# Kernel optimization log

Measured on AMD Instinct MI355X. Metric: run time of the kernel, lower is better.

The kernel has to match this reference:

```python
import jax, jax.numpy as jnp
import numpy as np

CLASSES = (16, 16)
CH_IN = 128
CH_LAT = 128
B, H, W = 1, 192, 256


def setup_inputs() -> dict:
    key = jax.random.key(0)
    ks = jax.random.split(key, 20)

    def w(k, shape, fan_in):
        return (jax.random.normal(k, shape, jnp.float32) / np.float32(np.sqrt(fan_in)))

    c0, c1 = CLASSES
    inp = {
        "x_in": jax.random.normal(ks[0], (B, CH_IN, H, W), jnp.float32),
        # 1x1 convs: weight [out, in], bias [out]
        "w_c11": w(ks[1], (CH_LAT, CH_IN), CH_IN), "b_c11": 0.01 * jax.random.normal(ks[2], (CH_LAT,), jnp.float32),
        "w_c12": w(ks[3], (CH_LAT, CH_LAT), CH_LAT), "b_c12": 0.01 * jax.random.normal(ks[4], (CH_LAT,), jnp.float32),
        "w_c13": w(ks[5], (c0 + 1, CH_LAT), CH_LAT), "b_c13": 0.01 * jax.random.normal(ks[6], (c0 + 1,), jnp.float32),
        # CondMul: weight [n_classes, in, out], bias [n_classes, out]
        "w_c21": w(ks[7], (c0, CH_IN, 32), CH_IN), "b_c21": 0.01 * jax.random.normal(ks[8], (c0, 32), jnp.float32),
        "w_c22": w(ks[9], (c0, 32, 32), 32), "b_c22": 0.01 * jax.random.normal(ks[10], (c0, 32), jnp.float32),
        "w_c23": w(ks[11], (c0, 32, c1), 32), "b_c23": 0.01 * jax.random.normal(ks[12], (c0, c1), jnp.float32),
        "w_r11": w(ks[13], (c0 * c1, CH_IN, 32), CH_IN), "b_r11": 0.01 * jax.random.normal(ks[14], (c0 * c1, 32), jnp.float32),
        "w_r12": w(ks[15], (c0 * c1, 32, 16), 32), "b_r12": 0.01 * jax.random.normal(ks[16], (c0 * c1, 16), jnp.float32),
        "w_r13": w(ks[17], (c0 * c1, 16, 1), 16), "b_r13": 0.01 * jax.random.normal(ks[18], (c0 * c1, 1), jnp.float32),
    }
    return inp


def _conv1x1(x, w, b):
    # x: [B,C,H,W], w: [O,C] -> [B,O,H,W]
    return jnp.einsum('bchw,oc->bohw', x, w) + b[None, :, None, None]


def _cond_mul(x, inds, w, b):
    # x: [N,in], inds: [N] int32, w: [C,in,out], b: [C,out] -> [N,out]
    return jnp.einsum('ni,nio->no', x, w[inds]) + b[inds]


def reference(x_in, w_c11, b_c11, w_c12, b_c12, w_c13, b_c13,
              w_c21, b_c21, w_c22, b_c22, w_c23, b_c23,
              w_r11, b_r11, w_r12, b_r12, w_r13, b_r13):
    lrelu = jax.nn.leaky_relu  # negative_slope=0.01, matches F.leaky_relu default
    c0, c1 = CLASSES
    total = c0 * c1

    x1 = lrelu(_conv1x1(x_in, w_c11, b_c11))
    x1 = lrelu(_conv1x1(x1, w_c12, b_c12))
    x1 = _conv1x1(x1, w_c13, b_c13)  # [B, c0+1, H, W]
    mask = lrelu(x1[:, -1:, :, :])

    # coarse routing: argmax over class logits, flattened in (B,H,W) order as in torch
    inds1 = jnp.argmax(x1[:, :c0], axis=1).reshape(-1).astype(jnp.int32)

    # tokens flattened via transpose(1,3): (B,W,H) order, faithful to original
    tok = jnp.transpose(x_in, (0, 3, 2, 1)).reshape(-1, x_in.shape[1])  # [N, CH_IN]

    x2 = lrelu(_cond_mul(tok, inds1, w_c21, b_c21))
    x2 = lrelu(_cond_mul(x2, inds1, w_c22, b_c22))
    x2 = _cond_mul(x2, inds1, w_c23, b_c23)  # [N, c1]

    inds2 = jnp.argmax(x2, axis=1).astype(jnp.int32)
    inds12 = inds1 * c0 + inds2  # original multiplies by classes[0]

    x3 = lrelu(_cond_mul(tok, inds12, w_r11, b_r11))
    x3 = lrelu(_cond_mul(x3, inds12, w_r12, b_r12))
    r = _cond_mul(x3, inds12, w_r13, b_r13).reshape(-1)  # [N]

    x_real = (inds12.astype(jnp.float32) + r) * (1.0 / float(total))
    x_real = x_real.reshape(x_in.shape[0], 1, x_in.shape[2], x_in.shape[3])
    return x_real, mask
```

## Files before the change

### kernel.cpp

```cpp
#include <hip/hip_runtime.h>

#define NPIX 49152
#define H_ 192
#define W_ 256
#define TPB 64

__global__ __launch_bounds__(256) void wtrans2_k(const float* __restrict__ Wa,
    float* __restrict__ WTa, const float* __restrict__ Wb,
    float* __restrict__ WTb, int* __restrict__ S) {
  const int b = blockIdx.x;
  const float* __restrict__ W = (b < 16) ? Wa : Wb;
  float* __restrict__ WT = (b < 16) ? WTa : WTb;
  const int bb = b & 15;
  __shared__ float tile[32][33];
  const int bx = bb & 3, by = bb >> 2;
  const int c = threadIdx.x & 31, r0 = threadIdx.x >> 5;
#pragma unroll
  for (int j = 0; j < 4; ++j) {
    const int r = r0 + j * 8;
    tile[r][c] = W[(by * 32 + r) * 128 + bx * 32 + c];
  }
  __syncthreads();
#pragma unroll
  for (int j = 0; j < 4; ++j) {
    const int r = r0 + j * 8;
    WT[(bx * 32 + r) * 128 + by * 32 + c] = tile[c][r];
  }
  if (b == 0) {
    const int t = threadIdx.x;
    if (t < 32) S[t] = 0;
    S[1088 + t] = 0;
    S[1344 + t] = 0;
  }
}

__global__ __launch_bounds__(512) void convfused_k(const float* __restrict__ X,
    const float* __restrict__ WT1, const float* __restrict__ Bv1,
    const float* __restrict__ WT2, const float* __restrict__ Bv2,
    const float* __restrict__ W3, const float* __restrict__ Bv3,
    unsigned char* __restrict__ inds1, float* __restrict__ mask_out,
    int* __restrict__ cnt1, float* __restrict__ xt) {
  __shared__ float xs2[128][65];
  __shared__ float w3s[128 * 20];
  __shared__ int lh[16];
  const int t = threadIdx.x;
  const int px = t & 63;
  const int p0 = blockIdx.x * 64;
  int ob = (t >> 6) * 16;
  ob = __builtin_amdgcn_readfirstlane(ob);
  if (t < 16) lh[t] = 0;

  {
    float xr[16];
#pragma unroll
    for (int kk = 0; kk < 16; ++kk)
      xr[kk] = X[(ob + kk) * NPIX + p0 + px];
#pragma unroll
    for (int kk = 0; kk < 16; ++kk)
      xs2[ob + kk][px] = xr[kk];
  }
  __syncthreads();

  float acc[16];

  const float* __restrict__ W1u = WT1 + ob;
#pragma unroll
  for (int o = 0; o < 16; ++o) acc[o] = Bv1[ob + o];
#pragma unroll 8
  for (int k = 0; k < 128; ++k) {
    const float xv = xs2[k][px];
#pragma unroll
    for (int o = 0; o < 16; ++o)
      acc[o] = fmaf(xv, W1u[k * 128 + o], acc[o]);
  }

#pragma unroll
  for (int i = 0; i < 4; ++i) {
    const int idx = t * 4 + i;
    const int tok = idx >> 5, c4 = idx & 31;
    const int pg = p0 + tok;
    float4 v;
    v.x = xs2[c4 * 4 + 0][tok];
    v.y = xs2[c4 * 4 + 1][tok];
    v.z = xs2[c4 * 4 + 2][tok];
    v.w = xs2[c4 * 4 + 3][tok];
    *(float4*)(xt + ((pg & 255) * H_ + (pg >> 8)) * 128 + c4 * 4) = v;
  }
  __syncthreads();

#pragma unroll
  for (int o = 0; o < 16; ++o) {
    const float v = acc[o];
    xs2[ob + o][px] = v > 0.f ? v : 0.01f * v;
  }
  __syncthreads();

  const float* __restrict__ W2u = WT2 + ob;
#pragma unroll
  for (int o = 0; o < 16; ++o) acc[o] = Bv2[ob + o];
#pragma unroll 8
  for (int k = 0; k < 128; ++k) {
    const float xv = xs2[k][px];
#pragma unroll
    for (int o = 0; o < 16; ++o)
      acc[o] = fmaf(xv, W2u[k * 128 + o], acc[o]);
  }
  __syncthreads();

#pragma unroll
  for (int o = 0; o < 16; ++o) {
    const float v = acc[o];
    xs2[ob + o][px] = v > 0.f ? v : 0.01f * v;
  }
  for (int i = t; i < 17 * 128; i += 512)
    w3s[(i & 127) * 20 + (i >> 7)] = W3[i];
  __syncthreads();

  {
    const int p = t >> 3, s = t & 7;
    float s2[2];
    s2[0] = Bv3[2 * s];
    s2[1] = Bv3[2 * s + 1];
    float m = Bv3[16];
#pragma unroll 8
    for (int k = 0; k < 128; ++k) {
      const float xv = xs2[k][p];
      float2 w2 = *(const float2*)&w3s[k * 20 + 2 * s];
      s2[0] = fmaf(xv, w2.x, s2[0]);
      s2[1] = fmaf(xv, w2.y, s2[1]);
      m = fmaf(xv, w3s[k * 20 + 16], m);
    }
    float bv = s2[0];
    int bi = 2 * s;
    if (s2[1] > bv) { bv = s2[1]; bi = 2 * s + 1; }
#pragma unroll
    for (int d = 1; d < 8; d <<= 1) {
      const float ov = __shfl_xor(bv, d, 64);
      const int oi = __shfl_xor(bi, d, 64);
      if (ov > bv || (ov == bv && oi < bi)) { bv = ov; bi = oi; }
    }
    if (s == 0) {
      inds1[p0 + p] = (unsigned char)bi;
      mask_out[p0 + p] = m > 0.f ? m : 0.01f * m;
      atomicAdd(&lh[bi], 1);
    }
  }
  __syncthreads();
  if (t < 16 && lh[t] > 0) atomicAdd(&cnt1[t], lh[t]);
}

template<typename T>
__global__ __launch_bounds__(256) void scatter_k(const T* __restrict__ bins,
    const int* __restrict__ cnt, int* __restrict__ cursor,
    int* __restrict__ ord, int nbins) {
  __shared__ int loff[256], lhist[256], lbase[256], lcur[256];
  __shared__ int wsC[4];
  const int t = threadIdx.x;
  const int lane = t & 63, wvi = t >> 6;
  const int c = (t < nbins) ? cnt[t] : 0;
  int ic = c;
  for (int d = 1; d < 64; d <<= 1) {
    const int u = __shfl_up(ic, d, 64);
    if (lane >= d) ic += u;
  }
  if (lane == 63) wsC[wvi] = ic;
  if (t < nbins) { lhist[t] = 0; lcur[t] = 0; }
  __syncthreads();
  int bc = 0;
#pragma unroll
  for (int w2 = 0; w2 < 4; ++w2) if (w2 < wvi) bc += wsC[w2];
  ic += bc;
  if (t < nbins) loff[t] = ic - c;
  __syncthreads();
  const int n = blockIdx.x * 256 + t;
  const int b = (int)bins[n];
  atomicAdd(&lhist[b], 1);
  __syncthreads();
  if (t < nbins && lhist[t] > 0) lbase[t] = atomicAdd(&cursor[t], lhist[t]);
  __syncthreads();
  const int r = atomicAdd(&lcur[b], 1);
  ord[loff[b] + lbase[b] + r] = n;
}

__global__ __launch_bounds__(256) void chain1_k(const float* __restrict__ xt,
    const int* __restrict__ ord1, const int* __restrict__ cnt1,
    const float* __restrict__ wc21, const float* __restrict__ bc21,
    const float* __restrict__ wc22, const float* __restrict__ bc22,
    const float* __restrict__ wc23, const float* __restrict__ bc23,
    int* __restrict__ e12a, int* __restrict__ cnt2) {
  __shared__ float w1s[4096];
  __shared__ float w2s[1024];
  __shared__ float w3s[512];
  __shared__ float bs[80];
  __shared__ float xs_[64][132];
  __shared__ int lh[16];
  __shared__ int sel[4];
  __shared__ int wsC[4], wsD[4];
  const int t = threadIdx.x;
  const int lane = t & 63, wvi = t >> 6;
  if (t == 0) sel[0] = -1;
  if (t < 16) lh[t] = 0;
  {
    const int cb = (t < 16) ? cnt1[t] : 0;
    const int nb = (cb + TPB - 1) / TPB;
    int ic = cb, id = nb;
    for (int d = 1; d < 64; d <<= 1) {
      const int uc = __shfl_up(ic, d, 64);
      const int ud = __shfl_up(id, d, 64);
      if (lane >= d) { ic += uc; id += ud; }
    }
    if (lane == 63) { wsC[wvi] = ic; wsD[wvi] = id; }
    __syncthreads();
    int bc = 0, bd = 0;
#pragma unroll
    for (int w2 = 0; w2 < 4; ++w2) {
      if (w2 < wvi) { bc += wsC[w2]; bd += wsD[w2]; }
    }
    ic += bc; id += bd;
    const int accB = id - nb, accO = ic - cb;
    if (t < 16 && (int)blockIdx.x >= accB && (int)blockIdx.x < accB + nb) {
      sel[0] = t; sel[1] = blockIdx.x - accB; sel[2] = accO; sel[3] = cb;
    }
  }
  __syncthreads();
  if (sel[0] < 0) return;
  const int e     = __builtin_amdgcn_readfirstlane(sel[0]);
  const int chunk = __builtin_amdgcn_readfirstlane(sel[1]);
  const int offe  = __builtin_amdgcn_readfirstlane(sel[2]);
  const int cnt   = __builtin_amdgcn_readfirstlane(sel[3]);

  const int tg = t >> 2, sub = t & 3;
  const int l0 = (t & 63) & ~3;
  const int pos = chunk * TPB + tg;
  const bool valid = pos < cnt;
  const int n = valid ? ord1[offe + pos] : 0;

  {
    const float4* __restrict__ Wg1 = (const float4*)(wc21 + e * 4096);
#pragma unroll
    for (int j = 0; j < 4; ++j)
      *(float4*)&w1s[t * 4 + j * 1024] = Wg1[t + j * 256];
    const float4* __restrict__ Wg2 = (const float4*)(wc22 + e * 1024);
    *(float4*)&w2s[t * 4] = Wg2[t];
    if (t < 128) {
      const float4* __restrict__ Wg3 = (const float4*)(wc23 + e * 512);
      *(float4*)&w3s[t * 4] = Wg3[t];
    }
    if (t < 32) bs[t] = bc21[e * 32 + t];
    else if (t < 64) bs[t] = bc22[e * 32 + (t - 32)];
    else if (t < 80) bs[t] = bc23[e * 16 + (t - 64)];
  }
  {
    const float4* __restrict__ src = (const float4*)(xt + n * 128 + sub * 32);
    float4 tmp[8];
#pragma unroll
    for (int j = 0; j < 8; ++j) tmp[j] = src[j];
#pragma unroll
    for (int j = 0; j < 8; ++j)
      *(float4*)(&xs_[tg][sub * 32 + 4 * j]) = tmp[j];
  }
  __syncthreads();

  const int wb1 = sub * 8;
  float a[8];
#pragma unroll
  for (int o = 0; o < 8; ++o) a[o] = bs[wb1 + o];
#pragma unroll
  for (int k = 0; k < 128; k += 4) {
    float x4[4];
    *(float4*)x4 = *(const float4*)(&xs_[tg][k]);
#pragma unroll
    for (int kk = 0; kk < 4; ++kk) {
      float w8[8];
      *(float4*)&w8[0] = *(const float4*)&w1s[(k + kk) * 32 + wb1];
      *(float4*)&w8[4] = *(const float4*)&w1s[(k + kk) * 32 + wb1 + 4];
#pragma unroll
      for (int o = 0; o < 8; ++o) a[o] = fmaf(x4[kk], w8[o], a[o]);
    }
  }
#pragma unroll
  for (int o = 0; o < 8; ++o) a[o] = a[o] > 0.f ? a[o] : 0.01f * a[o];

  float b[8];
#pragma unroll
  for (int o = 0; o < 8; ++o) b[o] = bs[32 + wb1 + o];
#pragma unroll
  for (int i = 0; i < 32; ++i) {
    const float hv = __shfl(a[i & 7], l0 + (i >> 3), 64);
    float w8[8];
    *(float4*)&w8[0] = *(const float4*)&w2s[i * 32 + wb1];
    *(float4*)&w8[4] = *(const float4*)&w2s[i * 32 + wb1 + 4];
#pragma unroll
    for (int o = 0; o < 8; ++o) b[o] = fmaf(hv, w8[o], b[o]);
  }
#pragma unroll
  for (int o = 0; o < 8; ++o) b[o] = b[o] > 0.f ? b[o] : 0.01f * b[o];

  float s[4];
#pragma unroll
  for (int j = 0; j < 4; ++j) s[j] = bs[64 + sub * 4 + j];
#pragma unroll
  for (int i = 0; i < 32; ++i) {
    const float hv = __shfl(b[i & 7], l0 + (i >> 3), 64);
    float w4[4];
    *(float4*)w4 = *(const float4*)&w3s[i * 16 + sub * 4];
#pragma unroll
    for (int j = 0; j < 4; ++j) s[j] = fmaf(hv, w4[j], s[j]);
  }

  float bv = s[0];
  int bi = sub * 4;
#pragma unroll
  for (int j = 1; j < 4; ++j) {
    if (s[j] > bv) { bv = s[j]; bi = sub * 4 + j; }
  }
#pragma unroll
  for (int d = 1; d < 4; d <<= 1) {
    const float ov = __shfl_xor(bv, d, 64);
    const int oi = __shfl_xor(bi, d, 64);
    if (ov > bv || (ov == bv && oi < bi)) { bv = ov; bi = oi; }
  }
  const int e12 = e * 16 + bi;
  if (valid && sub == 0) {
    e12a[n] = e12;
    atomicAdd(&lh[bi], 1);
  }
  __syncthreads();
  if (t < 16 && lh[t] > 0)
    atomicAdd(&cnt2[e * 16 + t], lh[t]);
}

__global__ __launch_bounds__(256) void chain2_k(const float* __restrict__ xt,
    const int* __restrict__ ord2, const int* __restrict__ cnt2,
    const float* __restrict__ wr11, const float* __restrict__ br11,
    const float* __restrict__ wr12, const float* __restrict__ br12,
    const float* __restrict__ wr13, const float* __restrict__ br13,
    float* __restrict__ out) {
  __shared__ float w1s[4096];
  __shared__ float w2s[512];
  __shared__ float w3s[16];
  __shared__ float bs[49];
  __shared__ float xs_[64][132];
  __shared__ int sel[4];
  __shared__ int wsC[4], wsD[4];
  const int t = threadIdx.x;
  const int lane = t & 63, wvi = t >> 6;
  if (t == 0) sel[0] = -1;
  {
    const int cb = cnt2[t];
    const int nb = (cb + TPB - 1) / TPB;
    int ic = cb, id = nb;
    for (int d = 1; d < 64; d <<= 1) {
      const int uc = __shfl_up(ic, d, 64);
      const int ud = __shfl_up(id, d, 64);
      if (lane >= d) { ic += uc; id += ud; }
    }
    if (lane == 63) { wsC[wvi] = ic; wsD[wvi] = id; }
    __syncthreads();
    int bc = 0, bd = 0;
#pragma unroll
    for (int w2 = 0; w2 < 4; ++w2) {
      if (w2 < wvi) { bc += wsC[w2]; bd += wsD[w2]; }
    }
    ic += bc; id += bd;
    const int accB = id - nb, accO = ic - cb;
    if ((int)blockIdx.x >= accB && (int)blockIdx.x < accB + nb) {
      sel[0] = t; sel[1] = blockIdx.x - accB; sel[2] = accO; sel[3] = cb;
    }
  }
  __syncthreads();
  if (sel[0] < 0) return;
  const int e12   = __builtin_amdgcn_readfirstlane(sel[0]);
  const int chunk = __builtin_amdgcn_readfirstlane(sel[1]);
  const int offe  = __builtin_amdgcn_readfirstlane(sel[2]);
  const int cnt   = __builtin_amdgcn_readfirstlane(sel[3]);

  const int tg = t >> 2, sub = t & 3;
  const int l0 = (t & 63) & ~3;
  const int pos = chunk * TPB + tg;
  const bool valid = pos < cnt;
  const int n = valid ? ord2[offe + pos] : 0;

  {
    const float4* __restrict__ Wg1 = (const float4*)(wr11 + e12 * 4096);
#pragma unroll
    for (int j = 0; j < 4; ++j)
      *(float4*)&w1s[t * 4 + j * 1024] = Wg1[t + j * 256];
    if (t < 128) {
      const float4* __restrict__ Wg2 = (const float4*)(wr12 + e12 * 512);
      *(float4*)&w2s[t * 4] = Wg2[t];
    }
    if (t < 16) w3s[t] = wr13[e12 * 16 + t];
    if (t < 32) bs[t] = br11[e12 * 32 + t];
    else if (t < 48) bs[t] = br12[e12 * 16 + (t - 32)];
    else if (t == 48) bs[48] = br13[e12];
  }
  {
    const float4* __restrict__ src = (const float4*)(xt + n * 128 + sub * 32);
    float4 tmp[8];
#pragma unroll
    for (int j = 0; j < 8; ++j) tmp[j] = src[j];
#pragma unroll
    for (int j = 0; j < 8; ++j)
      *(float4*)(&xs_[tg][sub * 32 + 4 * j]) = tmp[j];
  }
  __syncthreads();

  const int wb1 = sub * 8;
  float a[8];
#pragma unroll
  for (int o = 0; o < 8; ++o) a[o] = bs[wb1 + o];
#pragma unroll
  for (int k = 0; k < 128; k += 4) {
    float x4[4];
    *(float4*)x4 = *(const float4*)(&xs_[tg][k]);
#pragma unroll
    for (int kk = 0; kk < 4; ++kk) {
      float w8[8];
      *(float4*)&w8[0] = *(const float4*)&w1s[(k + kk) * 32 + wb1];
      *(float4*)&w8[4] = *(const float4*)&w1s[(k + kk) * 32 + wb1 + 4];
#pragma unroll
      for (int o = 0; o < 8; ++o) a[o] = fmaf(x4[kk], w8[o], a[o]);
    }
  }
#pragma unroll
  for (int o = 0; o < 8; ++o) a[o] = a[o] > 0.f ? a[o] : 0.01f * a[o];

  float s[4];
#pragma unroll
  for (int j = 0; j < 4; ++j) s[j] = bs[32 + sub * 4 + j];
#pragma unroll
  for (int i = 0; i < 32; ++i) {
    const float hv = __shfl(a[i & 7], l0 + (i >> 3), 64);
    float w4[4];
    *(float4*)w4 = *(const float4*)&w2s[i * 16 + sub * 4];
#pragma unroll
    for (int j = 0; j < 4; ++j) s[j] = fmaf(hv, w4[j], s[j]);
  }
#pragma unroll
  for (int j = 0; j < 4; ++j) s[j] = s[j] > 0.f ? s[j] : 0.01f * s[j];

  float r = bs[48];
#pragma unroll
  for (int i = 0; i < 16; ++i) {
    const float hv = __shfl(s[i & 3], l0 + (i >> 2), 64);
    r = fmaf(hv, w3s[i], r);
  }

  if (valid && sub == 0) out[n] = ((float)e12 + r) * (1.0f / 256.0f);
}

extern "C" void kernel_launch(void* const* d_in, const int* in_sizes, int n_in,
                              void* d_out, int out_size, void* d_ws,
                              size_t ws_size, hipStream_t stream) {
  const float* x_in  = (const float*)d_in[0];
  const float* w_c11 = (const float*)d_in[1];
  const float* b_c11 = (const float*)d_in[2];
  const float* w_c12 = (const float*)d_in[3];
  const float* b_c12 = (const float*)d_in[4];
  const float* w_c13 = (const float*)d_in[5];
  const float* b_c13 = (const float*)d_in[6];
  const float* w_c21 = (const float*)d_in[7];
  const float* b_c21 = (const float*)d_in[8];
  const float* w_c22 = (const float*)d_in[9];
  const float* b_c22 = (const float*)d_in[10];
  const float* w_c23 = (const float*)d_in[11];
  const float* b_c23 = (const float*)d_in[12];
  const float* w_r11 = (const float*)d_in[13];
  const float* b_r11 = (const float*)d_in[14];
  const float* w_r12 = (const float*)d_in[15];
  const float* b_r12 = (const float*)d_in[16];
  const float* w_r13 = (const float*)d_in[17];
  const float* b_r13 = (const float*)d_in[18];

  float* out = (float*)d_out;

  float* R0 = (float*)d_ws;
  float* R1 = R0 + 128 * NPIX;
  float* R2 = R1 + 128 * NPIX;

  float* xt = R0;
  unsigned char* inds1 = (unsigned char*)R2;
  float* wT1 = R2 + 12288;
  float* wT2 = wT1 + 16384;
  int* S = (int*)R2 + 45056;

  int* cnt1 = S;
  int* cur1 = S + 16;
  int* cnt2 = S + 1088;
  int* cur2 = S + 1344;

  int* ib   = (int*)R1;
  int* ord1 = ib;
  int* ord2 = ib + NPIX;
  int* e12a = ib + 2 * NPIX;

  wtrans2_k<<<32, 256, 0, stream>>>(w_c11, wT1, w_c12, wT2, S);
  convfused_k<<<NPIX / 64, 512, 0, stream>>>(x_in, wT1, b_c11, wT2, b_c12,
      w_c13, b_c13, inds1, out + NPIX, cnt1, xt);
  scatter_k<unsigned char><<<NPIX / 256, 256, 0, stream>>>(inds1, cnt1, cur1,
                                                           ord1, 16);
  chain1_k<<<NPIX / TPB + 16, 256, 0, stream>>>(xt, ord1, cnt1,
      w_c21, b_c21, w_c22, b_c22, w_c23, b_c23, e12a, cnt2);
  scatter_k<int><<<NPIX / 256, 256, 0, stream>>>(e12a, cnt2, cur2, ord2, 256);
  chain2_k<<<NPIX / TPB + 256, 256, 0, stream>>>(xt, ord2, cnt2,
      w_r11, b_r11, w_r12, b_r12, w_r13, b_r13, out);
}
```

Baseline: 115.3 us.

## Process 128 pixels per block in fused conv with channel-halved LDS staging

The fused 1x1 conv kernel now handles 128 pixels per block instead of 64, with each thread accumulating two pixels so every weight load feeds twice as many FMAs. To fit in shared memory, input channels and intermediate activations are staged in two 64-channel halves through a [64][130] buffer, which adds extra barriers. The final 17-output head is split over 4 lanes per pixel with float4 weight reads. The costs are doubled accumulator registers (possibly lower occupancy), half as many blocks, and more synchronization.

Result: slower. 123.3 us (+6.9%).

```diff
diff --git a/kernel.cpp b/kernel.cpp
--- a/kernel.cpp
+++ b/kernel.cpp
@@ -40,101 +40,229 @@
     const float* __restrict__ W3, const float* __restrict__ Bv3,
     unsigned char* __restrict__ inds1, float* __restrict__ mask_out,
     int* __restrict__ cnt1, float* __restrict__ xt) {
-  __shared__ float xs2[128][65];
+  __shared__ float xbuf[64][130];
   __shared__ float w3s[128 * 20];
   __shared__ int lh[16];
   const int t = threadIdx.x;
-  const int px = t & 63;
-  const int p0 = blockIdx.x * 64;
-  int ob = (t >> 6) * 16;
+  const int lane = t & 63;
+  const int wv = t >> 6;
+  const int p0 = blockIdx.x * 128;
+  int ob = wv * 16;
   ob = __builtin_amdgcn_readfirstlane(ob);
+  const int px0 = lane, px1 = lane + 64;
   if (t < 16) lh[t] = 0;
-
-  {
+  for (int i = t; i < 17 * 128; i += 512)
+    w3s[(i & 127) * 20 + (i >> 7)] = W3[i];
+
+  const float* __restrict__ W1u = WT1 + ob;
+  const float* __restrict__ W2u = WT2 + ob;
+  float acc1[32];
+#pragma unroll
+  for (int o = 0; o < 16; ++o) {
+    const float b = Bv1[ob + o];
+    acc1[2 * o] = b; acc1[2 * o + 1] = b;
+  }
+
+  {
+    const int rb = wv * 8;
     float xr[16];
 #pragma unroll
-    for (int kk = 0; kk < 16; ++kk)
-      xr[kk] = X[(ob + kk) * NPIX + p0 + px];
-#pragma unroll
-    for (int kk = 0; kk < 16; ++kk)
-      xs2[ob + kk][px] = xr[kk];
-  }
-  __syncthreads();
-
-  float acc[16];
-
-  const float* __restrict__ W1u = WT1 + ob;
-#pragma unroll
-  for (int o = 0; o < 16; ++o) acc[o] = Bv1[ob + o];
-#pragma unroll 8
-  for (int k = 0; k < 128; ++k) {
-    const float xv = xs2[k][px];
-#pragma unroll
-    for (int o = 0; o < 16; ++o)
-      acc[o] = fmaf(xv, W1u[k * 128 + o], acc[o]);
-  }
-
+    for (int j = 0; j < 8; ++j) {
+      xr[2 * j]     = X[(rb + j) * NPIX + p0 + px0];
+      xr[2 * j + 1] = X[(rb + j) * NPIX + p0 + px1];
+    }
+#pragma unroll
+    for (int j = 0; j < 8; ++j) {
+      xbuf[rb + j][px0] = xr[2 * j];
+      xbuf[rb + j][px1] = xr[2 * j + 1];
+    }
+  }
+  __syncthreads();
+
+#pragma unroll 4
+  for (int k = 0; k < 64; ++k) {
+    const float xa = xbuf[k][px0];
+    const float xb = xbuf[k][px1];
+#pragma unroll
+    for (int o = 0; o < 16; ++o) {
+      const float wgt = W1u[k * 128 + o];
+      acc1[2 * o]     = fmaf(xa, wgt, acc1[2 * o]);
+      acc1[2 * o + 1] = fmaf(xb, wgt, acc1[2 * o + 1]);
+    }
+  }
 #pragma unroll
   for (int i = 0; i < 4; ++i) {
     const int idx = t * 4 + i;
-    const int tok = idx >> 5, c4 = idx & 31;
+    const int tok = idx >> 4, c4 = idx & 15;
     const int pg = p0 + tok;
     float4 v;
-    v.x = xs2[c4 * 4 + 0][tok];
-    v.y = xs2[c4 * 4 + 1][tok];
-    v.z = xs2[c4 * 4 + 2][tok];
-    v.w = xs2[c4 * 4 + 3][tok];
+    v.x = xbuf[c4 * 4 + 0][tok];
+    v.y = xbuf[c4 * 4 + 1][tok];
+    v.z = xbuf[c4 * 4 + 2][tok];
+    v.w = xbuf[c4 * 4 + 3][tok];
     *(float4*)(xt + ((pg & 255) * H_ + (pg >> 8)) * 128 + c4 * 4) = v;
   }
   __syncthreads();
 
+  {
+    const int rb = wv * 8;
+    float xr[16];
+#pragma unroll
+    for (int j = 0; j < 8; ++j) {
+      xr[2 * j]     = X[(64 + rb + j) * NPIX + p0 + px0];
+      xr[2 * j + 1] = X[(64 + rb + j) * NPIX + p0 + px1];
+    }
+#pragma unroll
+    for (int j = 0; j < 8; ++j) {
+      xbuf[rb + j][px0] = xr[2 * j];
+      xbuf[rb + j][px1] = xr[2 * j + 1];
+    }
+  }
+  __syncthreads();
+
+#pragma unroll 4
+  for (int k = 64; k < 128; ++k) {
+    const float xa = xbuf[k - 64][px0];
+    const float xb = xbuf[k - 64][px1];
+#pragma unroll
+    for (int o = 0; o < 16; ++o) {
+      const float wgt = W1u[k * 128 + o];
+      acc1[2 * o]     = fmaf(xa, wgt, acc1[2 * o]);
+      acc1[2 * o + 1] = fmaf(xb, wgt, acc1[2 * o + 1]);
+    }
+  }
+#pragma unroll
+  for (int i = 0; i < 4; ++i) {
+    const int idx = t * 4 + i;
+    const int tok = idx >> 4, c4 = idx & 15;
+    const int pg = p0 + tok;
+    float4 v;
+    v.x = xbuf[c4 * 4 + 0][tok];
+    v.y = xbuf[c4 * 4 + 1][tok];
+    v.z = xbuf[c4 * 4 + 2][tok];
+    v.w = xbuf[c4 * 4 + 3][tok];
+    *(float4*)(xt + ((pg & 255) * H_ + (pg >> 8)) * 128 + 64 + c4 * 4) = v;
+  }
+  __syncthreads();
+
+  if (wv < 4) {
+    const int rb = wv * 16;
+#pragma unroll
+    for (int o = 0; o < 16; ++o) {
+      float va = acc1[2 * o], vb = acc1[2 * o + 1];
+      va = va > 0.f ? va : 0.01f * va;
+      vb = vb > 0.f ? vb : 0.01f * vb;
+      xbuf[rb + o][px0] = va;
+      xbuf[rb + o][px1] = vb;
+    }
+  }
+  __syncthreads();
+
+  float acc2[32];
 #pragma unroll
   for (int o = 0; o < 16; ++o) {
-    const float v = acc[o];
-    xs2[ob + o][px] = v > 0.f ? v : 0.01f * v;
-  }
-  __syncthreads();
-
-  const float* __restrict__ W2u = WT2 + ob;
-#pragma unroll
-  for (int o = 0; o < 16; ++o) acc[o] = Bv2[ob + o];
+    const float b = Bv2[ob + o];
+    acc2[2 * o] = b; acc2[2 * o + 1] = b;
+  }
+#pragma unroll 4
+  for (int k = 0; k < 64; ++k) {
+    const float xa = xbuf[k][px0];
+    const float xb = xbuf[k][px1];
+#pragma unroll
+    for (int o = 0; o < 16; ++o) {
+      const float wgt = W2u[k * 128 + o];
+      acc2[2 * o]     = fmaf(xa, wgt, acc2[2 * o]);
+      acc2[2 * o + 1] = fmaf(xb, wgt, acc2[2 * o + 1]);
+    }
+  }
+  __syncthreads();
+
+  if (wv >= 4) {
+    const int rb = (wv - 4) * 16;
+#pragma unroll
+    for (int o = 0; o < 16; ++o) {
+      float va = acc1[2 * o], vb = acc1[2 * o + 1];
+      va = va > 0.f ? va : 0.01f * va;
+      vb = vb > 0.f ? vb : 0.01f * vb;
+      xbuf[rb + o][px0] = va;
+      xbuf[rb + o][px1] = vb;
+    }
+  }
+  __syncthreads();
+
+#pragma unroll 4
+  for (int k = 64; k < 128; ++k) {
+    const float xa = xbuf[k - 64][px0];
+    const float xb = xbuf[k - 64][px1];
+#pragma unroll
+    for (int o = 0; o < 16; ++o) {
+      const float wgt = W2u[k * 128 + o];
+      acc2[2 * o]     = fmaf(xa, wgt, acc2[2 * o]);
+      acc2[2 * o + 1] = fmaf(xb, wgt, acc2[2 * o + 1]);
+    }
+  }
+  __syncthreads();
+
+  if (wv < 4) {
+    const int rb = wv * 16;
+#pragma unroll
+    for (int o = 0; o < 16; ++o) {
+      float va = acc2[2 * o], vb = acc2[2 * o + 1];
+      va = va > 0.f ? va : 0.01f * va;
+      vb = vb > 0.f ? vb : 0.01f * vb;
+      xbuf[rb + o][px0] = va;
+      xbuf[rb + o][px1] = vb;
+    }
+  }
+  __syncthreads();
+
+  const int p = t >> 2, s = t & 3;
+  float s4[4];
+#pragma unroll
+  for (int j = 0; j < 4; ++j) s4[j] = Bv3[s * 4 + j];
+  float m = Bv3[16];
 #pragma unroll 8
-  for (int k = 0; k < 128; ++k) {
-    const float xv = xs2[k][px];
-#pragma unroll
-    for (int o = 0; o < 16; ++o)
-      acc[o] = fmaf(xv, W2u[k * 128 + o], acc[o]);
-  }
-  __syncthreads();
-
-#pragma unroll
-  for (int o = 0; o < 16; ++o) {
-    const float v = acc[o];
-    xs2[ob + o][px] = v > 0.f ? v : 0.01f * v;
-  }
-  for (int i = t; i < 17 * 128; i += 512)
-    w3s[(i & 127) * 20 + (i >> 7)] = W3[i];
-  __syncthreads();
-
-  {
-    const int p = t >> 3, s = t & 7;
-    float s2[2];
-    s2[0] = Bv3[2 * s];
-    s2[1] = Bv3[2 * s + 1];
-    float m = Bv3[16];
+  for (int k = 0; k < 64; ++k) {
+    const float xv = xbuf[k][p];
+    float w4[4];
+    *(float4*)w4 = *(const float4*)&w3s[k * 20 + s * 4];
+#pragma unroll
+    for (int j = 0; j < 4; ++j) s4[j] = fmaf(xv, w4[j], s4[j]);
+    m = fmaf(xv, w3s[k * 20 + 16], m);
+  }
+  __syncthreads();
+
+  if (wv >= 4) {
+    const int rb = (wv - 4) * 16;
+#pragma unroll
+    for (int o = 0; o < 16; ++o) {
+      float va = acc2[2 * o], vb = acc2[2 * o + 1];
+      va = va > 0.f ? va : 0.01f * va;
+      vb = vb > 0.f ? vb : 0.01f * vb;
+      xbuf[rb + o][px0] = va;
+      xbuf[rb + o][px1] = vb;
+    }
+  }
+  __syncthreads();
+
 #pragma unroll 8
-    for (int k = 0; k < 128; ++k) {
-      const float xv = xs2[k][p];
-      float2 w2 = *(const float2*)&w3s[k * 20 + 2 * s];
-      s2[0] = fmaf(xv, w2.x, s2[0]);
-      s2[1] = fmaf(xv, w2.y, s2[1]);
-      m = fmaf(xv, w3s[k * 20 + 16], m);
-    }
-    float bv = s2[0];
-    int bi = 2 * s;
-    if (s2[1] > bv) { bv = s2[1]; bi = 2 * s + 1; }
-#pragma unroll
-    for (int d = 1; d < 8; d <<= 1) {
+  for (int k = 64; k < 128; ++k) {
+    const float xv = xbuf[k - 64][p];
+    float w4[4];
+    *(float4*)w4 = *(const float4*)&w3s[k * 20 + s * 4];
+#pragma unroll
+    for (int j = 0; j < 4; ++j) s4[j] = fmaf(xv, w4[j], s4[j]);
+    m = fmaf(xv, w3s[k * 20 + 16], m);
+  }
+  {
+    float bv = s4[0];
+    int bi = s * 4;
+#pragma unroll
+    for (int j = 1; j < 4; ++j) {
+      if (s4[j] > bv) { bv = s4[j]; bi = s * 4 + j; }
+    }
+#pragma unroll
+    for (int d = 1; d < 4; d <<= 1) {
       const float ov = __shfl_xor(bv, d, 64);
       const int oi = __shfl_xor(bi, d, 64);
       if (ov > bv || (ov == bv && oi < bi)) { bv = ov; bi = oi; }
@@ -496,7 +624,7 @@
   int* e12a = ib + 2 * NPIX;
 
   wtrans2_k<<<32, 256, 0, stream>>>(w_c11, wT1, w_c12, wT2, S);
-  convfused_k<<<NPIX / 64, 512, 0, stream>>>(x_in, wT1, b_c11, wT2, b_c12,
+  convfused_k<<<NPIX / 128, 512, 0, stream>>>(x_in, wT1, b_c11, wT2, b_c12,
       w_c13, b_c13, inds1, out + NPIX, cnt1, xt);
   scatter_k<unsigned char><<<NPIX / 256, 256, 0, stream>>>(inds1, cnt1, cur1,
                                                            ord1, 16);
```
